# Kernel optimization log

Hardware: AMD Instinct MI355X
Metric: run time of the kernel (lower is better)

The kernel has to match this reference:

```python
import jax, jax.numpy as jnp
import numpy as np

N_NODES = 100000
FEAT = 256
HID = 256
BATCH = 512
NUM_SAMPLES = [25, 10]  # layer_infos[0].num_samples, layer_infos[1].num_samples


def setup_inputs() -> dict:
    key = jax.random.key(0)
    ks = jax.random.split(key, 7)
    scale = 0.05
    return {
        "features": jax.random.normal(ks[0], (N_NODES, FEAT), dtype=jnp.float32),
        "adj": jax.random.randint(ks[1], (N_NODES, NUM_SAMPLES[0]), 0, N_NODES, dtype=jnp.int32),
        "batch": jax.random.randint(ks[2], (BATCH,), 0, N_NODES, dtype=jnp.int32),
        "W_self_0": jax.random.normal(ks[3], (FEAT, HID), dtype=jnp.float32) * scale,
        "W_neigh_0": jax.random.normal(ks[4], (FEAT, HID), dtype=jnp.float32) * scale,
        "W_self_1": jax.random.normal(ks[5], (HID, HID), dtype=jnp.float32) * scale,
        "W_neigh_1": jax.random.normal(ks[6], (HID, HID), dtype=jnp.float32) * scale,
    }


def reference(features, adj, batch, W_self_0, W_neigh_0, W_self_1, W_neigh_1):
    B = batch.shape[0]
    n_layers = 2
    # --- sample(): reverse-order neighbor expansion (deterministic: first-k slots) ---
    # hop 1 uses layer_infos[-1].num_samples = 10, hop 2 uses layer_infos[0].num_samples = 25
    s1 = adj[batch][:, : NUM_SAMPLES[1]].reshape(-1)  # [B*10]
    s2 = adj[s1][:, : NUM_SAMPLES[0]].reshape(-1)     # [B*250]
    support = [1, NUM_SAMPLES[1], NUM_SAMPLES[1] * NUM_SAMPLES[0]]  # [1, 10, 250]
    # --- gather input features per hop (irregular gather, memory bound) ---
    hidden = [features[batch], features[s1], features[s2]]
    Ws = [(W_self_0, W_neigh_0), (W_self_1, W_neigh_1)]
    for layer in range(n_layers):
        act = jax.nn.relu if layer < n_layers - 1 else (lambda x: x)
        W_s, W_n = Ws[layer]
        next_hidden = []
        for hop in range(n_layers - layer):
            n_smp = NUM_SAMPLES[n_layers - hop - 1]
            self_vecs = hidden[hop]  # [B*support[hop], d]
            neigh = hidden[hop + 1].reshape(B * support[hop], n_smp, -1)
            neigh_mean = neigh.mean(axis=1)  # mean aggregator
            # concat=False -> sum of self and neighbor transforms
            next_hidden.append(act(self_vecs @ W_s + neigh_mean @ W_n))
        hidden = next_hidden
    out = hidden[0]  # [B, HID]
    # GraphSAGE l2-normalizes final embeddings
    norm = jnp.maximum(jnp.linalg.norm(out, axis=1, keepdims=True), 1e-12)
    return out / norm
```

## Files before the change

### kernel.cpp

```cpp
#include <hip/hip_runtime.h>
#include <cstdint>
#include <cstddef>

#define NNODES 100000
#define FEATD  256
#define HIDD   256
#define NBATCH 512
#define FAN1   10
#define FAN2   25
#define NS1    (NBATCH*FAN1)
#define MTOT   (NBATCH+NS1)

typedef __attribute__((ext_vector_type(8))) short short8;
typedef __attribute__((ext_vector_type(4))) float f32x4;

__device__ __forceinline__ unsigned short f2bf(float f) {
    unsigned int u = __float_as_uint(f);
    unsigned int r = (u + 0x7fffu + ((u >> 16) & 1u)) >> 16;
    return (unsigned short)r;
}

__global__ __launch_bounds__(256) void k_wcvt(
    const float* __restrict__ Ws0, const float* __restrict__ Wn0,
    unsigned short* __restrict__ B0t) {
    __shared__ unsigned short Ts[64][72];
    const int t  = threadIdx.x;
    const int kt = blockIdx.x >> 2;
    const int nt = blockIdx.x & 3;
    const int k0 = kt * 64, n0 = nt * 64;
    const float* W = (k0 < 256) ? (Ws0 + (size_t)k0 * 256)
                                : (Wn0 + (size_t)(k0 - 256) * 256);
    #pragma unroll
    for (int i = 0; i < 4; ++i) {
        int s  = t + i * 256;
        int kr = s >> 4;
        int c4 = s & 15;
        float4 v = *reinterpret_cast<const float4*>(W + (size_t)kr * 256 + n0 + c4 * 4);
        Ts[c4 * 4 + 0][kr] = f2bf(v.x);
        Ts[c4 * 4 + 1][kr] = f2bf(v.y);
        Ts[c4 * 4 + 2][kr] = f2bf(v.z);
        Ts[c4 * 4 + 3][kr] = f2bf(v.w);
    }
    __syncthreads();
    #pragma unroll
    for (int i = 0; i < 2; ++i) {
        int s  = t + i * 256;
        int nl = s >> 3;
        int k8 = (s & 7) * 8;
        *reinterpret_cast<short8*>(B0t + (size_t)(n0 + nl) * 512 + k0 + k8) =
            *reinterpret_cast<const short8*>(&Ts[nl][k8]);
    }
}

__global__ __launch_bounds__(512) void k_gg0(
    const float* __restrict__ feat, const int* __restrict__ adj,
    const int* __restrict__ batch, const unsigned short* __restrict__ B0t,
    float* __restrict__ H0, float* __restrict__ H1) {
    __shared__ __align__(16) unsigned short As[16][520];
    __shared__ __align__(16) unsigned short Bs[256][72];
    const int t   = threadIdx.x;
    const int wv  = t >> 6;
    const int l   = t & 63;
    const int q   = l >> 4;
    const int m15 = l & 15;
    const int r0  = blockIdx.x * 16;
    const bool isBatch = (r0 < NBATCH);

    #pragma unroll
    for (int i = 0; i < 2; ++i) {
        const int r = wv * 2 + i;
        const int R = r0 + r;
        int node;
        if (isBatch) {
            node = batch[R];
        } else {
            int idx = R - NBATCH;
            int b   = idx / FAN1;
            int j   = idx - b * FAN1;
            node = adj[(size_t)batch[b] * FAN2 + j];
        }
        float4 selfv = *reinterpret_cast<const float4*>(
            feat + (size_t)node * FEATD + l * 4);
        const int* arow = adj + (size_t)node * FAN2;
        int myidx = (l < FAN2) ? arow[l] : 0;
        float4 acc = make_float4(0.f, 0.f, 0.f, 0.f);
        float s;
        if (isBatch) {
            #pragma unroll
            for (int k = 0; k < FAN1; ++k) {
                int nb = __shfl(myidx, k);
                float4 v = *reinterpret_cast<const float4*>(
                    feat + (size_t)nb * FEATD + l * 4);
                acc.x += v.x; acc.y += v.y; acc.z += v.z; acc.w += v.w;
            }
            s = 1.0f / (float)FAN1;
        } else {
            #pragma unroll
            for (int k = 0; k < FAN2; ++k) {
                int nb = __shfl(myidx, k);
                float4 v = *reinterpret_cast<const float4*>(
                    feat + (size_t)nb * FEATD + l * 4);
                acc.x += v.x; acc.y += v.y; acc.z += v.z; acc.w += v.w;
            }
            s = 1.0f / (float)FAN2;
        }
        acc.x *= s; acc.y *= s; acc.z *= s; acc.w *= s;
        ushort4 ps, pn;
        ps.x = f2bf(selfv.x); ps.y = f2bf(selfv.y);
        ps.z = f2bf(selfv.z); ps.w = f2bf(selfv.w);
        pn.x = f2bf(acc.x);   pn.y = f2bf(acc.y);
        pn.z = f2bf(acc.z);   pn.w = f2bf(acc.w);
        *reinterpret_cast<ushort4*>(&As[r][l * 4])       = ps;
        *reinterpret_cast<ushort4*>(&As[r][256 + l * 4]) = pn;
    }
    __syncthreads();

    f32x4 acc0 = (f32x4)0.f, acc1 = (f32x4)0.f;

    for (int kt = 0; kt < 8; ++kt) {
        const int kb = kt * 64;
        #pragma unroll
        for (int i = 0; i < 4; ++i) {
            int s  = t + i * 512;
            int nl = s >> 3;
            int k8 = (s & 7) * 8;
            *reinterpret_cast<short8*>(&Bs[nl][k8]) =
                *reinterpret_cast<const short8*>(
                    B0t + (size_t)nl * 512 + kb + k8);
        }
        __syncthreads();
        #pragma unroll
        for (int s2 = 0; s2 < 2; ++s2) {
            const int kk = s2 * 32 + q * 8;
            short8 a = *reinterpret_cast<const short8*>(&As[m15][kb + kk]);
            short8 b0 = *reinterpret_cast<const short8*>(&Bs[wv * 32 + m15][kk]);
            short8 b1 = *reinterpret_cast<const short8*>(&Bs[wv * 32 + 16 + m15][kk]);
            acc0 = __builtin_amdgcn_mfma_f32_16x16x32_bf16(a, b0, acc0, 0, 0, 0);
            acc1 = __builtin_amdgcn_mfma_f32_16x16x32_bf16(a, b1, acc1, 0, 0, 0);
        }
        __syncthreads();
    }

    #pragma unroll
    for (int f = 0; f < 2; ++f) {
        const int n = wv * 32 + f * 16 + m15;
        const f32x4& a = f ? acc1 : acc0;
        #pragma unroll
        for (int j = 0; j < 4; ++j) {
            int m = r0 + q * 4 + j;
            float v = fmaxf(a[j], 0.f);
            if (isBatch)
                H0[(size_t)m * HIDD + n] = v;
            else
                H1[(size_t)(m - NBATCH) * HIDD + n] = v;
        }
    }
}

__global__ __launch_bounds__(128) void k_layer1(
    const float* __restrict__ H0, const float* __restrict__ H1,
    const float* __restrict__ Ws, const float* __restrict__ Wn,
    float* __restrict__ out) {
    __shared__ float At[2][512];
    const int t  = threadIdx.x;
    const int rb = blockIdx.x * 2;

    {
        int r = t >> 6, c4 = t & 63;
        *reinterpret_cast<float4*>(&At[r][c4 * 4]) =
            *reinterpret_cast<const float4*>(H0 + (size_t)(rb + r) * HIDD + c4 * 4);
    }
    {
        int r = t >> 6, c4 = t & 63;
        const float* base = H1 + (size_t)(rb + r) * FAN1 * HIDD + c4 * 4;
        float4 acc = make_float4(0.f, 0.f, 0.f, 0.f);
        #pragma unroll
        for (int j = 0; j < FAN1; ++j) {
            float4 v = *reinterpret_cast<const float4*>(base + (size_t)j * HIDD);
            acc.x += v.x; acc.y += v.y; acc.z += v.z; acc.w += v.w;
        }
        const float s = 1.0f / (float)FAN1;
        acc.x *= s; acc.y *= s; acc.z *= s; acc.w *= s;
        *reinterpret_cast<float4*>(&At[r][256 + c4 * 4]) = acc;
    }
    __syncthreads();

    const int wv = t >> 6;
    const int tc = (t & 63) * 4;
    float4 acc = make_float4(0.f, 0.f, 0.f, 0.f);

    const float* Wh[2] = {Ws, Wn};
    #pragma unroll
    for (int half = 0; half < 2; ++half) {
        const float* W  = Wh[half] + tc;
        const int    ko = half * 256;
        for (int k4 = 0; k4 < 64; ++k4) {
            int k = k4 * 4;
            float4 a = *reinterpret_cast<const float4*>(&At[wv][ko + k]);
            const float* ap = &a.x;
            #pragma unroll
            for (int kk = 0; kk < 4; ++kk) {
                float4 w = *reinterpret_cast<const float4*>(W + (size_t)(k + kk) * HIDD);
                float av = ap[kk];
                acc.x += av * w.x; acc.y += av * w.y;
                acc.z += av * w.z; acc.w += av * w.w;
            }
        }
    }

    float p = acc.x*acc.x + acc.y*acc.y + acc.z*acc.z + acc.w*acc.w;
    #pragma unroll
    for (int off = 32; off >= 1; off >>= 1) p += __shfl_xor(p, off);
    float inv = 1.0f / fmaxf(sqrtf(p), 1e-12f);
    acc.x *= inv; acc.y *= inv; acc.z *= inv; acc.w *= inv;
    *reinterpret_cast<float4*>(out + (size_t)(rb + wv) * HIDD + tc) = acc;
}

extern "C" void kernel_launch(void* const* d_in, const int* in_sizes, int n_in,
                              void* d_out, int out_size, void* d_ws, size_t ws_size,
                              hipStream_t stream) {
    const float* feat  = (const float*)d_in[0];
    const int*   adj   = (const int*)d_in[1];
    const int*   batch = (const int*)d_in[2];
    const float* Ws0   = (const float*)d_in[3];
    const float* Wn0   = (const float*)d_in[4];
    const float* Ws1   = (const float*)d_in[5];
    const float* Wn1   = (const float*)d_in[6];
    float* out = (float*)d_out;

    char* ws = (char*)d_ws;
    unsigned short* B0t = (unsigned short*)(ws + 0);
    float*          H0  = (float*)(ws + 262144);
    float*          H1  = (float*)(ws + 786432);

    k_wcvt<<<32, 256, 0, stream>>>(Ws0, Wn0, B0t);
    k_gg0<<<MTOT / 16, 512, 0, stream>>>(feat, adj, batch, B0t, H0, H1);
    k_layer1<<<NBATCH / 2, 128, 0, stream>>>(H0, H1, Ws1, Wn1, out);
}
```

Before: 207.6 us.

## Use bf16 MFMA for layer 1, store hidden in bf16, drop LDS B staging

```diff
diff --git a/kernel.cpp b/kernel.cpp
--- a/kernel.cpp
+++ b/kernel.cpp
@@ -19,17 +19,26 @@
     unsigned int r = (u + 0x7fffu + ((u >> 16) & 1u)) >> 16;
     return (unsigned short)r;
 }
+__device__ __forceinline__ float bf2f(unsigned short h) {
+    return __uint_as_float(((unsigned int)h) << 16);
+}
 
 __global__ __launch_bounds__(256) void k_wcvt(
     const float* __restrict__ Ws0, const float* __restrict__ Wn0,
-    unsigned short* __restrict__ B0t) {
+    const float* __restrict__ Ws1, const float* __restrict__ Wn1,
+    unsigned short* __restrict__ B0t, unsigned short* __restrict__ B1t) {
     __shared__ unsigned short Ts[64][72];
-    const int t  = threadIdx.x;
-    const int kt = blockIdx.x >> 2;
-    const int nt = blockIdx.x & 3;
+    const int t     = threadIdx.x;
+    const int which = blockIdx.x >> 5;
+    const int loc   = blockIdx.x & 31;
+    const int kt = loc >> 2, nt = loc & 3;
     const int k0 = kt * 64, n0 = nt * 64;
-    const float* W = (k0 < 256) ? (Ws0 + (size_t)k0 * 256)
-                                : (Wn0 + (size_t)(k0 - 256) * 256);
+    const float* W;
+    if (which == 0)
+        W = (k0 < 256) ? (Ws0 + (size_t)k0 * 256) : (Wn0 + (size_t)(k0 - 256) * 256);
+    else
+        W = (k0 < 256) ? (Ws1 + (size_t)k0 * 256) : (Wn1 + (size_t)(k0 - 256) * 256);
+    unsigned short* Bt = which ? B1t : B0t;
     #pragma unroll
     for (int i = 0; i < 4; ++i) {
         int s  = t + i * 256;
@@ -47,7 +56,7 @@
         int s  = t + i * 256;
         int nl = s >> 3;
         int k8 = (s & 7) * 8;
-        *reinterpret_cast<short8*>(B0t + (size_t)(n0 + nl) * 512 + k0 + k8) =
+        *reinterpret_cast<short8*>(Bt + (size_t)(n0 + nl) * 512 + k0 + k8) =
             *reinterpret_cast<const short8*>(&Ts[nl][k8]);
     }
 }
@@ -55,9 +64,8 @@
 __global__ __launch_bounds__(512) void k_gg0(
     const float* __restrict__ feat, const int* __restrict__ adj,
     const int* __restrict__ batch, const unsigned short* __restrict__ B0t,
-    float* __restrict__ H0, float* __restrict__ H1) {
+    unsigned short* __restrict__ H0, unsigned short* __restrict__ H1) {
     __shared__ __align__(16) unsigned short As[16][520];
-    __shared__ __align__(16) unsigned short Bs[256][72];
     const int t   = threadIdx.x;
     const int wv  = t >> 6;
     const int l   = t & 63;
@@ -116,29 +124,20 @@
     __syncthreads();
 
     f32x4 acc0 = (f32x4)0.f, acc1 = (f32x4)0.f;
-
+    const unsigned short* b0p = B0t + (size_t)(wv * 32 + m15) * 512;
+    const unsigned short* b1p = B0t + (size_t)(wv * 32 + 16 + m15) * 512;
+    #pragma unroll
     for (int kt = 0; kt < 8; ++kt) {
         const int kb = kt * 64;
         #pragma unroll
-        for (int i = 0; i < 4; ++i) {
-            int s  = t + i * 512;
-            int nl = s >> 3;
-            int k8 = (s & 7) * 8;
-            *reinterpret_cast<short8*>(&Bs[nl][k8]) =
-                *reinterpret_cast<const short8*>(
-                    B0t + (size_t)nl * 512 + kb + k8);
-        }
-        __syncthreads();
-        #pragma unroll
         for (int s2 = 0; s2 < 2; ++s2) {
-            const int kk = s2 * 32 + q * 8;
-            short8 a = *reinterpret_cast<const short8*>(&As[m15][kb + kk]);
-            short8 b0 = *reinterpret_cast<const short8*>(&Bs[wv * 32 + m15][kk]);
-            short8 b1 = *reinterpret_cast<const short8*>(&Bs[wv * 32 + 16 + m15][kk]);
+            const int kk = kb + s2 * 32 + q * 8;
+            short8 a  = *reinterpret_cast<const short8*>(&As[m15][kk]);
+            short8 b0 = *reinterpret_cast<const short8*>(b0p + kk);
+            short8 b1 = *reinterpret_cast<const short8*>(b1p + kk);
             acc0 = __builtin_amdgcn_mfma_f32_16x16x32_bf16(a, b0, acc0, 0, 0, 0);
             acc1 = __builtin_amdgcn_mfma_f32_16x16x32_bf16(a, b1, acc1, 0, 0, 0);
         }
-        __syncthreads();
     }
 
     #pragma unroll
@@ -148,7 +147,7 @@
         #pragma unroll
         for (int j = 0; j < 4; ++j) {
             int m = r0 + q * 4 + j;
-            float v = fmaxf(a[j], 0.f);
+            unsigned short v = f2bf(fmaxf(a[j], 0.f));
             if (isBatch)
                 H0[(size_t)m * HIDD + n] = v;
             else
@@ -157,63 +156,79 @@
     }
 }
 
-__global__ __launch_bounds__(128) void k_layer1(
-    const float* __restrict__ H0, const float* __restrict__ H1,
-    const float* __restrict__ Ws, const float* __restrict__ Wn,
-    float* __restrict__ out) {
-    __shared__ float At[2][512];
-    const int t  = threadIdx.x;
-    const int rb = blockIdx.x * 2;
+__global__ __launch_bounds__(512) void k_l1(
+    const unsigned short* __restrict__ H0, const unsigned short* __restrict__ H1,
+    const unsigned short* __restrict__ B1t, float* __restrict__ out) {
+    __shared__ __align__(16) unsigned short As[16][520];
+    __shared__ float rn[16][8];
+    const int t   = threadIdx.x;
+    const int wv  = t >> 6;
+    const int l   = t & 63;
+    const int q   = l >> 4;
+    const int m15 = l & 15;
+    const int rb  = blockIdx.x * 16;
 
     {
-        int r = t >> 6, c4 = t & 63;
-        *reinterpret_cast<float4*>(&At[r][c4 * 4]) =
-            *reinterpret_cast<const float4*>(H0 + (size_t)(rb + r) * HIDD + c4 * 4);
+        int r = t >> 5, c8 = (t & 31) * 8;
+        *reinterpret_cast<short8*>(&As[r][c8]) =
+            *reinterpret_cast<const short8*>(H0 + (size_t)(rb + r) * HIDD + c8);
     }
     {
-        int r = t >> 6, c4 = t & 63;
-        const float* base = H1 + (size_t)(rb + r) * FAN1 * HIDD + c4 * 4;
-        float4 acc = make_float4(0.f, 0.f, 0.f, 0.f);
+        int r = t >> 5, c8 = (t & 31) * 8;
+        const unsigned short* base = H1 + (size_t)(rb + r) * FAN1 * HIDD + c8;
+        float a[8];
+        #pragma unroll
+        for (int e = 0; e < 8; ++e) a[e] = 0.f;
         #pragma unroll
         for (int j = 0; j < FAN1; ++j) {
-            float4 v = *reinterpret_cast<const float4*>(base + (size_t)j * HIDD);
-            acc.x += v.x; acc.y += v.y; acc.z += v.z; acc.w += v.w;
-        }
-        const float s = 1.0f / (float)FAN1;
-        acc.x *= s; acc.y *= s; acc.z *= s; acc.w *= s;
-        *reinterpret_cast<float4*>(&At[r][256 + c4 * 4]) = acc;
-    }
-    __syncthreads();
-
-    const int wv = t >> 6;
-    const int tc = (t & 63) * 4;
-    float4 acc = make_float4(0.f, 0.f, 0.f, 0.f);
-
-    const float* Wh[2] = {Ws, Wn};
-    #pragma unroll
-    for (int half = 0; half < 2; ++half) {
-        const float* W  = Wh[half] + tc;
-        const int    ko = half * 256;
-        for (int k4 = 0; k4 < 64; ++k4) {
-            int k = k4 * 4;
-            float4 a = *reinterpret_cast<const float4*>(&At[wv][ko + k]);
-            const float* ap = &a.x;
+            short8 v = *reinterpret_cast<const short8*>(base + (size_t)j * HIDD);
             #pragma unroll
-            for (int kk = 0; kk < 4; ++kk) {
-                float4 w = *reinterpret_cast<const float4*>(W + (size_t)(k + kk) * HIDD);
-                float av = ap[kk];
-                acc.x += av * w.x; acc.y += av * w.y;
-                acc.z += av * w.z; acc.w += av * w.w;
-            }
-        }
-    }
-
-    float p = acc.x*acc.x + acc.y*acc.y + acc.z*acc.z + acc.w*acc.w;
-    #pragma unroll
-    for (int off = 32; off >= 1; off >>= 1) p += __shfl_xor(p, off);
-    float inv = 1.0f / fmaxf(sqrtf(p), 1e-12f);
-    acc.x *= inv; acc.y *= inv; acc.z *= inv; acc.w *= inv;
-    *reinterpret_cast<float4*>(out + (size_t)(rb + wv) * HIDD + tc) = acc;
+            for (int e = 0; e < 8; ++e) a[e] += bf2f((unsigned short)v[e]);
+        }
+        short8 p;
+        #pragma unroll
+        for (int e = 0; e < 8; ++e) p[e] = (short)f2bf(a[e] * (1.0f / FAN1));
+        *reinterpret_cast<short8*>(&As[r][256 + c8]) = p;
+    }
+    __syncthreads();
+
+    f32x4 acc0 = (f32x4)0.f, acc1 = (f32x4)0.f;
+    const unsigned short* b0p = B1t + (size_t)(wv * 32 + m15) * 512;
+    const unsigned short* b1p = B1t + (size_t)(wv * 32 + 16 + m15) * 512;
+    #pragma unroll
+    for (int kt = 0; kt < 8; ++kt) {
+        const int kb = kt * 64;
+        #pragma unroll
+        for (int s2 = 0; s2 < 2; ++s2) {
+            const int kk = kb + s2 * 32 + q * 8;
+            short8 a  = *reinterpret_cast<const short8*>(&As[m15][kk]);
+            short8 b0 = *reinterpret_cast<const short8*>(b0p + kk);
+            short8 b1 = *reinterpret_cast<const short8*>(b1p + kk);
+            acc0 = __builtin_amdgcn_mfma_f32_16x16x32_bf16(a, b0, acc0, 0, 0, 0);
+            acc1 = __builtin_amdgcn_mfma_f32_16x16x32_bf16(a, b1, acc1, 0, 0, 0);
+        }
+    }
+
+    #pragma unroll
+    for (int j = 0; j < 4; ++j) {
+        float p = acc0[j] * acc0[j] + acc1[j] * acc1[j];
+        p += __shfl_xor(p, 1);
+        p += __shfl_xor(p, 2);
+        p += __shfl_xor(p, 4);
+        p += __shfl_xor(p, 8);
+        if (m15 == 0) rn[q * 4 + j][wv] = p;
+    }
+    __syncthreads();
+
+    #pragma unroll
+    for (int j = 0; j < 4; ++j) {
+        const int m = q * 4 + j;
+        float s = rn[m][0] + rn[m][1] + rn[m][2] + rn[m][3]
+                + rn[m][4] + rn[m][5] + rn[m][6] + rn[m][7];
+        float inv = 1.0f / fmaxf(sqrtf(s), 1e-12f);
+        out[(size_t)(rb + m) * HIDD + wv * 32 + m15]      = acc0[j] * inv;
+        out[(size_t)(rb + m) * HIDD + wv * 32 + 16 + m15] = acc1[j] * inv;
+    }
 }
 
 extern "C" void kernel_launch(void* const* d_in, const int* in_sizes, int n_in,
@@ -230,10 +245,11 @@
 
     char* ws = (char*)d_ws;
     unsigned short* B0t = (unsigned short*)(ws + 0);
-    float*          H0  = (float*)(ws + 262144);
-    float*          H1  = (float*)(ws + 786432);
-
-    k_wcvt<<<32, 256, 0, stream>>>(Ws0, Wn0, B0t);
+    unsigned short* B1t = (unsigned short*)(ws + 262144);
+    unsigned short* H0  = (unsigned short*)(ws + 524288);
+    unsigned short* H1  = (unsigned short*)(ws + 786432);
+
+    k_wcvt<<<64, 256, 0, stream>>>(Ws0, Wn0, Ws1, Wn1, B0t, B1t);
     k_gg0<<<MTOT / 16, 512, 0, stream>>>(feat, adj, batch, B0t, H0, H1);
-    k_layer1<<<NBATCH / 2, 128, 0, stream>>>(H0, H1, Ws1, Wn1, out);
-}
+    k_l1<<<NBATCH / 16, 512, 0, stream>>>(H0, H1, B1t, out);
+}
```

New measurement: 192.5 us. 7.3% less time.
